# Kernel optimization log

Measured on AMD Instinct MI355X. Metric: run time of the kernel, lower is better.

## Reference

```python
import jax, jax.numpy as jnp
import numpy as np

B, H, W, C = 32, 64, 64, 64
F = 128
KH = KW = 3
SH = SW = 1
P = KH * KW * C  # flattened patch size = 576


def _glorot(key, shape):
    fan_in = KH * KW * C
    fan_out = KH * KW * F
    limit = np.sqrt(6.0 / (fan_in + fan_out)).astype(np.float32)
    return jax.random.uniform(key, shape, jnp.float32, -limit, limit)


def setup_inputs() -> dict:
    key = jax.random.key(0)
    k1, k2, k3 = jax.random.split(key, 3)
    inputs = jax.random.normal(k1, (B, H, W, C), dtype=jnp.float32)
    kernel = _glorot(k2, (KH, KW, C, F))
    control_points = _glorot(k3, (KH, KW, C, F))
    bias = jnp.zeros((F,), dtype=jnp.float32)
    return {"inputs": inputs, "kernel": kernel, "bias": bias, "control_points": control_points}


def _extract_patches(x):
    # SAME padding, stride 1; TF extract_patches ordering: (kh, kw, C), C fastest
    xp = jnp.pad(x, ((0, 0), (1, 1), (1, 1), (0, 0)))
    patches = jnp.stack(
        [xp[:, i:i + H, j:j + W, :] for i in range(KH) for j in range(KW)],
        axis=3,
    )  # [B, H, W, KH*KW, C]
    return patches.reshape(B, H, W, P)


def reference(inputs, kernel, bias, control_points):
    conv_out = jax.lax.conv_general_dilated(
        inputs, kernel, (SH, SW), "SAME",
        dimension_numbers=("NHWC", "HWIO", "NHWC"),
    )  # [B, H, W, F]

    # RBF branch via ||a-b||^2 = ||a||^2 + ||b||^2 - 2 a.b
    p = _extract_patches(inputs).reshape(-1, P)        # [N, P]
    c = control_points.reshape(P, F)                   # [P, F]
    pn = jnp.sum(p * p, axis=1, keepdims=True)         # [N, 1]
    cn = jnp.sum(c * c, axis=0)                        # [F]
    d = pn + cn - 2.0 * (p @ c)                        # [N, F] squared distances
    gamma = 1.0 / (2.0 * jnp.mean(d))                  # global mean over all patches/filters
    kan = jnp.exp(-gamma * d).reshape(B, H, W, F)

    return conv_out + kan + bias
```

## Files before the change

kernel.cpp:

```cpp
#include <hip/hip_runtime.h>


#define B_ 32
#define H_ 64
#define W_ 64
#define C_ 64
#define F_ 128
#define P_ 576
#define NPIX (B_*H_*W_)
#define NF   (NPIX*F_)

typedef __bf16  bf16x8 __attribute__((ext_vector_type(8)));
typedef float   f32x4  __attribute__((ext_vector_type(4)));

union BFU { __bf16 h; ushort s; };
union PKU { __bf16 h[2]; uint u; };

__device__ __forceinline__ ushort f2bf(float f) { BFU q; q.h = (__bf16)f; return q.s; }
__device__ __forceinline__ uint pk(float a, float b) {
    PKU q; q.h[0] = (__bf16)a; q.h[1] = (__bf16)b; return q.u;
}

__device__ __forceinline__ void gll16(const void* g, void* l) {
    __builtin_amdgcn_global_load_lds((const __attribute__((address_space(1))) void*)g,
                                     (__attribute__((address_space(3))) void*)l, 16, 0, 0);
}

__global__ void k_prep(const float* __restrict__ in, const float* __restrict__ wgt,
                       const float* __restrict__ ctrl, ushort* __restrict__ wsB,
                       float* __restrict__ cn, float* __restrict__ accum,
                       float* __restrict__ spn, float* __restrict__ spc) {
    __shared__ __attribute__((aligned(16))) float sh[1024];
    __shared__ float tabL[576];
    __shared__ float shs[4], shp[4];
    const int t = threadIdx.x;

    if (blockIdx.x < 288) {
        int e = blockIdx.x * 256 + t;
        int p = e >> 7, f = e & 127;
        int kc = p >> 6, r = p & 63;
        int ks = r >> 5, quad = (r >> 3) & 3, j = r & 7;
        int ntg = f >> 4, l16 = f & 15;
        int off0 = (kc * 2 + ks) * 8192 + ntg * 512 + (quad * 16 + l16) * 8 + j;
        wsB[off0]        = f2bf(wgt[e]);
        wsB[off0 + 4096] = f2bf(ctrl[e]);
        return;
    }
    if (blockIdx.x == 288) {
        int col = t & 31, pc8 = t >> 5;
        f32x4 a = {0.f, 0.f, 0.f, 0.f};
        const float* base = ctrl + col * 4;
        #pragma unroll 4
        for (int p = pc8 * 72; p < pc8 * 72 + 72; ++p) {
            f32x4 v = *(const f32x4*)(base + p * F_);
            a += v * v;
        }
        f32x4* sh4 = (f32x4*)sh;
        sh4[t] = a;
        __syncthreads();
        f32x4 s = {0.f, 0.f, 0.f, 0.f};
        if (t < 32) {
            #pragma unroll
            for (int q = 0; q < 8; ++q) s += sh4[q * 32 + t];
            *(f32x4*)(cn + t * 4) = s;
        }
        float tot = s.x + s.y + s.z + s.w;
        if (t < 64) {
            #pragma unroll
            for (int off = 32; off >= 1; off >>= 1) tot += __shfl_down(tot, off, 64);
            if (t == 0) accum[0] = tot;
        }
        return;
    }

    const int sb = blockIdx.x - 289;
    for (int e = t; e < 576; e += 256) {
        const f32x4* row = (const f32x4*)(ctrl + e * F_);
        f32x4 a = {0.f, 0.f, 0.f, 0.f};
        #pragma unroll 8
        for (int q = 0; q < 32; ++q) a += row[q];
        sh[e] = a.x + a.y + a.z + a.w;
    }
    __syncthreads();
    for (int idx = t; idx < 576; idx += 256) {
        int q = idx >> 6, c = idx & 63;
        int ry = q / 3, rx = q - 3 * ry;
        int my = (ry == 0) ? 3 : (ry == 2) ? 6 : 7;
        int mx = (rx == 0) ? 3 : (rx == 2) ? 6 : 7;
        float s = 0.f;
        #pragma unroll
        for (int ki = 0; ki < 3; ++ki)
            #pragma unroll
            for (int kj = 0; kj < 3; ++kj)
                if ((my >> ki & 1) && (mx >> kj & 1))
                    s += sh[(ki * 3 + kj) * 64 + c];
        tabL[idx] = s;
    }
    __syncthreads();

    const int seg = t & 15, grp = t >> 4;
    float s = 0.f, pc = 0.f;
    #pragma unroll 4
    for (int it = 0; it < 16; ++it) {
        int pix = sb * 256 + it * 16 + grp;
        int y = (pix >> 6) & 63, x = pix & 63;
        float4 v = *((const float4*)(in + pix * 64) + seg);
        int ry = (y == 0) ? 0 : (y == 63) ? 2 : 1;
        int rx = (x == 0) ? 0 : (x == 63) ? 2 : 1;
        float4 tv = *((const float4*)(tabL + (ry * 3 + rx) * 64) + seg);
        float wq = (float)((3 - (y == 0) - (y == 63)) * (3 - (x == 0) - (x == 63)));
        s  += wq * (v.x*v.x + v.y*v.y + v.z*v.z + v.w*v.w);
        pc += v.x*tv.x + v.y*tv.y + v.z*tv.z + v.w*tv.w;
    }
    #pragma unroll
    for (int off = 32; off >= 1; off >>= 1) {
        s  += __shfl_down(s,  off, 64);
        pc += __shfl_down(pc, off, 64);
    }
    if ((t & 63) == 0) { shs[t >> 6] = s; shp[t >> 6] = pc; }
    __syncthreads();
    if (t == 0)  spn[sb] = shs[0] + shs[1] + shs[2] + shs[3];
    if (t == 64) spc[sb] = shp[0] + shp[1] + shp[2] + shp[3];
}

__launch_bounds__(512, 4)
__global__ void k_main(const float* __restrict__ in, const ushort* __restrict__ wsB,
                       const float* __restrict__ bias, const float* __restrict__ cn,
                       const float* __restrict__ accum, const float* __restrict__ spn,
                       const float* __restrict__ spc, float* __restrict__ out) {
    __shared__ __attribute__((aligned(16))) ushort smem[34592];
    ushort* lI   = smem;
    ushort* lB   = smem + 17408;
    float*  sArr = (float*)(smem + 33792);
    float*  pnAr = (float*)(smem + 34336);

    const int tid = threadIdx.x;
    const int n0  = blockIdx.x * 128;
    const int b   = n0 >> 12;
    const int y0  = (n0 >> 6) & 63;
    const float* inb = in + b * 262144;

    const int w     = tid >> 6, lane = tid & 63;
    const int fq    = w & 3, mhalf = w >> 2;
    const int quad  = lane >> 4, l16 = lane & 15;

    {
        const char* src = (const char*)wsB + tid * 16;
        char* dst = (char*)lB + tid * 16;
        gll16(src, dst);
        gll16(src + 8192, dst + 8192);
    }

    for (int g = tid; g < 2176; g += 512) {
        int row4 = g / 544;
        int rem  = g - row4 * 544;
        int px = rem >> 3, c = rem & 7;
        int y = y0 + row4 - 1, x = px - 1;
        float4 v0 = make_float4(0.f, 0.f, 0.f, 0.f), v1 = v0;
        if (y >= 0 && y < 64 && x >= 0 && x < 64) {
            const float* sp = inb + y * 4096 + x * 64 + c * 8;
            v0 = *(const float4*)sp;
            v1 = *(const float4*)(sp + 4);
        }
        uint4 o = { pk(v0.x, v0.y), pk(v0.z, v0.w), pk(v1.x, v1.y), pk(v1.z, v1.w) };
        *(uint4*)&lI[(row4 * 68 + px) * 64 + ((c ^ (px & 7)) << 3)] = o;
        float s8 = v0.x*v0.x + v0.y*v0.y + v0.z*v0.z + v0.w*v0.w
                 + v1.x*v1.x + v1.y*v1.y + v1.z*v1.z + v1.w*v1.w;
        s8 += __shfl_xor(s8, 1, 64);
        s8 += __shfl_xor(s8, 2, 64);
        s8 += __shfl_xor(s8, 4, 64);
        if ((g & 7) == 0) sArr[row4 * 68 + px] = s8;
    }
    __syncthreads();

    if (tid < 128) {
        int yr = tid >> 6, x = tid & 63;
        float a = 0.f;
        #pragma unroll
        for (int dr = 0; dr < 3; ++dr)
            #pragma unroll
            for (int dc = 0; dc < 3; ++dc)
                a += sArr[(yr + dr) * 68 + x + dc];
        pnAr[tid] = a;
    }

    f32x4 accW[4][2], accC[4][2];
    #pragma unroll
    for (int mt = 0; mt < 4; ++mt)
        #pragma unroll
        for (int nt = 0; nt < 2; ++nt) {
            accW[mt][nt] = (f32x4){0.f, 0.f, 0.f, 0.f};
            accC[mt][nt] = (f32x4){0.f, 0.f, 0.f, 0.f};
        }

    const int fq2 = fq * 2;
    int cur = 0;
    #pragma unroll 1
    for (int t18 = 0; t18 < 18; ++t18) {
        const int kc = t18 >> 1, ks = t18 & 1;
        const int ki = (kc >= 6) ? 2 : (kc >= 3) ? 1 : 0;
        const int kj = kc - 3 * ki;

        if (t18 < 17) {
            const char* src = (const char*)wsB + (t18 + 1) * 16384 + tid * 16;
            char* dst = (char*)lB + ((cur ^ 1) * 16384) + tid * 16;
            gll16(src, dst);
            gll16(src + 8192, dst + 8192);
        }

        const ushort* lBc = lB + cur * 8192;
        bf16x8 bw[2], bc[2];
        #pragma unroll
        for (int nt = 0; nt < 2; ++nt) {
            bw[nt] = *(const bf16x8*)&lBc[(fq2 + nt) * 512 + lane * 8];
            bc[nt] = *(const bf16x8*)&lBc[4096 + (fq2 + nt) * 512 + lane * 8];
        }
        const int swk = (l16 + kj) & 7;
        const int rb0 = (mhalf + ki) * 68 + l16 + kj;
        const int sw  = ((ks * 4 + quad) ^ swk) << 3;
        __builtin_amdgcn_s_setprio(1);
        #pragma unroll
        for (int mt = 0; mt < 4; ++mt) {
            bf16x8 a = *(const bf16x8*)&lI[(rb0 + mt * 16) * 64 + sw];
            #pragma unroll
            for (int nt = 0; nt < 2; ++nt) {
                accW[mt][nt] = __builtin_amdgcn_mfma_f32_16x16x32_bf16(a, bw[nt], accW[mt][nt], 0, 0, 0);
                accC[mt][nt] = __builtin_amdgcn_mfma_f32_16x16x32_bf16(a, bc[nt], accC[mt][nt], 0, 0, 0);
            }
        }
        __builtin_amdgcn_s_setprio(0);
        if (t18 < 17) __syncthreads();
        cur ^= 1;
    }

    float sp = 0.f, sc = 0.f;
    #pragma unroll
    for (int q = 0; q < 8; ++q) {
        sp += spn[q * 64 + lane];
        sc += spc[q * 64 + lane];
    }
    #pragma unroll
    for (int off = 32; off >= 1; off >>= 1) {
        sp += __shfl_xor(sp, off, 64);
        sc += __shfl_xor(sc, off, 64);
    }
    float Sd = 128.f * sp + 131072.f * accum[0] - 2.f * sc;
    float g  = 0.5f * 16777216.f / Sd;
    float bv[2], cv[2];
    #pragma unroll
    for (int nt = 0; nt < 2; ++nt) {
        int gf = fq * 32 + nt * 16 + l16;
        bv[nt] = bias[gf];
        cv[nt] = cn[gf];
    }
    #pragma unroll
    for (int mt = 0; mt < 4; ++mt) {
        int rloc = mhalf * 64 + mt * 16 + quad * 4;
        float pv[4];
        #pragma unroll
        for (int r = 0; r < 4; ++r) pv[r] = pnAr[rloc + r];
        int gm = n0 + rloc;
        #pragma unroll
        for (int nt = 0; nt < 2; ++nt) {
            int gf = fq * 32 + nt * 16 + l16;
            #pragma unroll
            for (int r = 0; r < 4; ++r) {
                float d = pv[r] + cv[nt] - 2.f * accC[mt][nt][r];
                out[(gm + r) * F_ + gf] = accW[mt][nt][r] + bv[nt] + __expf(-g * d);
            }
        }
    }
}

extern "C" void kernel_launch(void* const* d_in, const int* in_sizes, int n_in,
                              void* d_out, int out_size, void* d_ws, size_t ws_size,
                              hipStream_t stream) {
    const float* in   = (const float*)d_in[0];
    const float* wgt  = (const float*)d_in[1];
    const float* bias = (const float*)d_in[2];
    const float* ctrl = (const float*)d_in[3];
    float* out = (float*)d_out;

    char* ws = (char*)d_ws;
    ushort* wsB   = (ushort*)(ws + 0);
    float*  cn    = (float*) (ws + 294912);
    float*  accum = (float*) (ws + 295424);
    float*  spn   = (float*) (ws + 295488);
    float*  spc   = (float*) (ws + 297536);

    k_prep <<<801,        256, 0, stream>>>(in, wgt, ctrl, wsB, cn, accum, spn, spc);
    k_main <<<NPIX / 128, 512, 0, stream>>>(in, wsB, bias, cn, accum, spn, spc, out);
}
```

Measured before the change: 150.5 us.

## Split gamma reduction into separate kernel and hand-tune main loop barriers

Prep work is split up. The 3x3 edge-sum table is now computed once into global memory, and a new k_gamma kernel computes the per-block patch-norm and cross-term partials. Before, each of 512 blocks recomputed the table from ctrl. In k_main, the __syncthreads around the double-buffered B-tile loads become explicit vmcnt waits plus raw s_barrier with sched_barrier fences, and the setprio hints are removed. This tightens synchronisation in the MFMA loop but adds a third kernel launch.

After: 146.8 us. 1.03x faster.

```diff
diff --git a/kernel.cpp b/kernel.cpp
--- a/kernel.cpp
+++ b/kernel.cpp
@@ -26,13 +26,10 @@
                                      (__attribute__((address_space(3))) void*)l, 16, 0, 0);
 }
 
-__global__ void k_prep(const float* __restrict__ in, const float* __restrict__ wgt,
-                       const float* __restrict__ ctrl, ushort* __restrict__ wsB,
-                       float* __restrict__ cn, float* __restrict__ accum,
-                       float* __restrict__ spn, float* __restrict__ spc) {
+__global__ void k_prep(const float* __restrict__ wgt, const float* __restrict__ ctrl,
+                       ushort* __restrict__ wsB, float* __restrict__ cn,
+                       float* __restrict__ accum, float* __restrict__ tab) {
     __shared__ __attribute__((aligned(16))) float sh[1024];
-    __shared__ float tabL[576];
-    __shared__ float shs[4], shp[4];
     const int t = threadIdx.x;
 
     if (blockIdx.x < 288) {
@@ -73,7 +70,6 @@
         return;
     }
 
-    const int sb = blockIdx.x - 289;
     for (int e = t; e < 576; e += 256) {
         const f32x4* row = (const f32x4*)(ctrl + e * F_);
         f32x4 a = {0.f, 0.f, 0.f, 0.f};
@@ -94,20 +90,24 @@
             for (int kj = 0; kj < 3; ++kj)
                 if ((my >> ki & 1) && (mx >> kj & 1))
                     s += sh[(ki * 3 + kj) * 64 + c];
-        tabL[idx] = s;
-    }
-    __syncthreads();
-
-    const int seg = t & 15, grp = t >> 4;
+        tab[idx] = s;
+    }
+}
+
+__launch_bounds__(256)
+__global__ void k_gamma(const float* __restrict__ in, const float* __restrict__ tab,
+                        float* __restrict__ spn, float* __restrict__ spc) {
+    __shared__ float shs[4], shp[4];
+    const int t = threadIdx.x, seg = t & 15, grp = t >> 4;
     float s = 0.f, pc = 0.f;
     #pragma unroll 4
     for (int it = 0; it < 16; ++it) {
-        int pix = sb * 256 + it * 16 + grp;
+        int pix = blockIdx.x * 256 + it * 16 + grp;
         int y = (pix >> 6) & 63, x = pix & 63;
         float4 v = *((const float4*)(in + pix * 64) + seg);
         int ry = (y == 0) ? 0 : (y == 63) ? 2 : 1;
         int rx = (x == 0) ? 0 : (x == 63) ? 2 : 1;
-        float4 tv = *((const float4*)(tabL + (ry * 3 + rx) * 64) + seg);
+        float4 tv = *((const float4*)(tab + (ry * 3 + rx) * 64) + seg);
         float wq = (float)((3 - (y == 0) - (y == 63)) * (3 - (x == 0) - (x == 63)));
         s  += wq * (v.x*v.x + v.y*v.y + v.z*v.z + v.w*v.w);
         pc += v.x*tv.x + v.y*tv.y + v.z*tv.z + v.w*tv.w;
@@ -119,8 +119,8 @@
     }
     if ((t & 63) == 0) { shs[t >> 6] = s; shp[t >> 6] = pc; }
     __syncthreads();
-    if (t == 0)  spn[sb] = shs[0] + shs[1] + shs[2] + shs[3];
-    if (t == 64) spc[sb] = shp[0] + shp[1] + shp[2] + shp[3];
+    if (t == 0)  spn[blockIdx.x] = shs[0] + shs[1] + shs[2] + shs[3];
+    if (t == 64) spc[blockIdx.x] = shp[0] + shp[1] + shp[2] + shp[3];
 }
 
 __launch_bounds__(512, 4)
@@ -206,7 +206,13 @@
             char* dst = (char*)lB + ((cur ^ 1) * 16384) + tid * 16;
             gll16(src, dst);
             gll16(src + 8192, dst + 8192);
-        }
+            asm volatile("s_waitcnt vmcnt(2)" ::: "memory");
+        } else {
+            asm volatile("s_waitcnt vmcnt(0)" ::: "memory");
+        }
+        __builtin_amdgcn_sched_barrier(0);
+        __builtin_amdgcn_s_barrier();
+        __builtin_amdgcn_sched_barrier(0);
 
         const ushort* lBc = lB + cur * 8192;
         bf16x8 bw[2], bc[2];
@@ -218,7 +224,6 @@
         const int swk = (l16 + kj) & 7;
         const int rb0 = (mhalf + ki) * 68 + l16 + kj;
         const int sw  = ((ks * 4 + quad) ^ swk) << 3;
-        __builtin_amdgcn_s_setprio(1);
         #pragma unroll
         for (int mt = 0; mt < 4; ++mt) {
             bf16x8 a = *(const bf16x8*)&lI[(rb0 + mt * 16) * 64 + sw];
@@ -228,8 +233,11 @@
                 accC[mt][nt] = __builtin_amdgcn_mfma_f32_16x16x32_bf16(a, bc[nt], accC[mt][nt], 0, 0, 0);
             }
         }
-        __builtin_amdgcn_s_setprio(0);
-        if (t18 < 17) __syncthreads();
+        __builtin_amdgcn_sched_barrier(0);
+        if (t18 < 17) {
+            __builtin_amdgcn_s_barrier();
+            __builtin_amdgcn_sched_barrier(0);
+        }
         cur ^= 1;
     }
 
@@ -285,9 +293,11 @@
     ushort* wsB   = (ushort*)(ws + 0);
     float*  cn    = (float*) (ws + 294912);
     float*  accum = (float*) (ws + 295424);
-    float*  spn   = (float*) (ws + 295488);
-    float*  spc   = (float*) (ws + 297536);
-
-    k_prep <<<801,        256, 0, stream>>>(in, wgt, ctrl, wsB, cn, accum, spn, spc);
-    k_main <<<NPIX / 128, 512, 0, stream>>>(in, wsB, bias, cn, accum, spn, spc, out);
-}
+    float*  tab   = (float*) (ws + 295488);
+    float*  spn   = (float*) (ws + 297792);
+    float*  spc   = (float*) (ws + 299840);
+
+    k_prep  <<<290,        256, 0, stream>>>(wgt, ctrl, wsB, cn, accum, tab);
+    k_gamma <<<NPIX / 256, 256, 0, stream>>>(in, tab, spn, spc);
+    k_main  <<<NPIX / 128, 512, 0, stream>>>(in, wsB, bias, cn, accum, spn, spc, out);
+}
```
